# Kernel tuning notes

Hardware: AMD Instinct MI355X
Metric: run time of the kernel (lower is better)

## Reference

```python
import jax, jax.numpy as jnp
import numpy as np

N_RAYS = 1_048_576
T_ITERS = 4
N_POINTS = 8
DIM = 64
N_LAYERS = 2
INF = 1e9


def setup_inputs() -> dict:
    key = jax.random.key(0)
    ks = jax.random.split(key, 12)
    orig = jax.random.normal(ks[0], (N_RAYS, 3), jnp.float32)
    vec = jax.random.normal(ks[1], (N_RAYS, 3), jnp.float32)
    masks = jax.random.bernoulli(ks[2], 0.6, (T_ITERS, N_RAYS))
    bbox_idxs = jax.random.randint(ks[3], (T_ITERS, N_RAYS), 0, 1024, jnp.int32)
    t1 = jax.random.uniform(ks[4], (T_ITERS, N_RAYS), jnp.float32) * 2.0
    t2 = t1 + jax.random.uniform(ks[5], (T_ITERS, N_RAYS), jnp.float32) * 2.0
    mesh_min = jnp.array([-1.0, -1.0, -1.0], jnp.float32)
    mesh_max = jnp.array([1.0, 1.0, 1.0], jnp.float32)
    s = 0.05
    W0 = jax.random.normal(ks[6], (3 * N_POINTS, DIM), jnp.float32) * s
    b0 = jnp.zeros((DIM,), jnp.float32)
    ln_g = jnp.ones((N_LAYERS, DIM), jnp.float32)
    ln_b = jnp.zeros((N_LAYERS, DIM), jnp.float32)
    Ws = jax.random.normal(ks[7], (N_LAYERS, DIM, DIM), jnp.float32) * s
    bs = jnp.zeros((N_LAYERS, DIM), jnp.float32)
    Wc = jax.random.normal(ks[8], (DIM,), jnp.float32) * s
    bc = jnp.zeros((), jnp.float32)
    Wd = jax.random.normal(ks[9], (DIM,), jnp.float32) * s
    bd = jnp.zeros((), jnp.float32)
    return dict(orig=orig, vec=vec, masks=masks, bbox_idxs=bbox_idxs, t1=t1, t2=t2,
                mesh_min=mesh_min, mesh_max=mesh_max, W0=W0, b0=b0,
                ln_g=ln_g, ln_b=ln_b, Ws=Ws, bs=bs, Wc=Wc, bc=bc, Wd=Wd, bd=bd)


def _layernorm(x, g, b):
    mu = jnp.mean(x, axis=-1, keepdims=True)
    var = jnp.mean((x - mu) ** 2, axis=-1, keepdims=True)
    return (x - mu) * jax.lax.rsqrt(var + 1e-5) * g + b


def _net_forward(x, W0, b0, ln_g, ln_b, Ws, bs, Wc, bc, Wd, bd):
    # x: [N, 3*n_points]
    y = x @ W0 + b0
    for i in range(N_LAYERS):
        y = jax.nn.relu(y)
        y = _layernorm(y, ln_g[i], ln_b[i])
        y = y @ Ws[i] + bs[i]
    y = jax.nn.relu(y)
    cls = y @ Wc + bc   # [N]
    dist = y @ Wd + bd  # [N]
    return cls, dist


def reference(orig, vec, masks, bbox_idxs, t1, t2, mesh_min, mesh_max,
              W0, b0, ln_g, ln_b, Ws, bs, Wc, bc, Wd, bd):
    n_rays = orig.shape[0]
    ts = jnp.linspace(0.0, 1.0, N_POINTS, dtype=jnp.float32)
    min_infl = mesh_min - 0.5 * (mesh_max - mesh_min)
    max_infl = mesh_max + 0.5 * (mesh_max - mesh_min)
    scale = max_infl - min_infl
    dist = jnp.full((n_rays,), INF, jnp.float32)
    for it in range(T_ITERS):
        mask, ct1, ct2 = masks[it], t1[it], t2[it]
        inp_orig = orig + vec * ct1[:, None]          # [N,3]
        inp_vec = vec * (ct2 - ct1)[:, None]          # [N,3]
        # sample n_points along segment: [N, P, 3]
        inp = inp_orig[:, None, :] + inp_vec[:, None, :] * ts[None, :, None]
        inp = (inp - min_infl) / scale
        x = inp.reshape(n_rays, -1)                   # [N, 3P]
        hit_c, dv_c = _net_forward(x, W0, b0, ln_g, ln_b, Ws, bs, Wc, bc, Wd, bd)
        hit = jnp.where(mask, hit_c, 0.0)             # masked_scatter_ equivalent
        dv = jnp.where(mask, dv_c, 0.0) + ct1
        upd = (hit > 0) & (dv < dist) & mask
        dist = jnp.where(upd, dv, dist)
    dist = jnp.where(dist == INF, 0.0, dist)
    return (dist > 0, dist)
```

## Files before the change

### kernel.cpp

```cpp
#include <hip/hip_runtime.h>
#include <hip/hip_bf16.h>
#include <stdint.h>

#define NRAYS 1048576
#define INFV  1e9f
#define TBIG  1e30f

typedef short short8 __attribute__((ext_vector_type(8)));
typedef float f32x4  __attribute__((ext_vector_type(4)));

#define WS_B0   16
#define FB0     1024
#define FB1     2048

#define PKLO(a,b) ((int)(((unsigned)(a) & 0xFFFFu) | ((unsigned)(b) << 16)))
#define PKHI(a,b) ((int)(((unsigned)(a) >> 16) | ((unsigned)(b) & 0xFFFF0000u)))

__device__ __forceinline__ float ldf(const void* p, int i, int fm) {
    if (fm) return ((const float*)p)[i];
    unsigned u = ((const unsigned short*)p)[i];
    return __uint_as_float(u << 16);
}

__device__ __forceinline__ void split3(float f, int& him, int& lo) {
    unsigned u = __float_as_uint(f);
    float r = f - __uint_as_float(u & 0xFFFF0000u);
    unsigned um = __float_as_uint(r);
    float r2 = r - __uint_as_float(um & 0xFFFF0000u);
    unsigned ul = __float_as_uint(r2);
    him = (int)((u >> 16) | (um & 0xFFFF0000u));
    lo  = (int)(ul >> 16);
}

__device__ __forceinline__ unsigned comp16(int h, float f) {
    unsigned u = __float_as_uint(f);
    if (h == 0) return u >> 16;
    float r = f - __uint_as_float(u & 0xFFFF0000u);
    unsigned um = __float_as_uint(r);
    if (h == 1) return um >> 16;
    float r2 = r - __uint_as_float(um & 0xFFFF0000u);
    return __float_as_uint(r2) >> 16;
}

__device__ __forceinline__ float rsum16(float x) {
    int v;
    v = __builtin_amdgcn_update_dpp(0, __float_as_int(x), 0x128, 0xF, 0xF, false); x += __int_as_float(v);
    v = __builtin_amdgcn_update_dpp(0, __float_as_int(x), 0x124, 0xF, 0xF, false); x += __int_as_float(v);
    v = __builtin_amdgcn_update_dpp(0, __float_as_int(x), 0x122, 0xF, 0xF, false); x += __int_as_float(v);
    v = __builtin_amdgcn_update_dpp(0, __float_as_int(x), 0x121, 0xF, 0xF, false); x += __int_as_float(v);
    return x;
}

union I4S8 { int4 i; short8 s; };
__device__ __forceinline__ short8 mk8i(int a, int b, int c, int d) {
    I4S8 u; u.i = make_int4(a, b, c, d); return u.s;
}
__device__ __forceinline__ short8 ld_frag(const unsigned* p) {
    I4S8 u; u.i = *(const int4*)p; return u.s;
}

__global__ __launch_bounds__(256) void conv_k(
    const void* __restrict__ mmin, const void* __restrict__ mmax,
    const void* __restrict__ masks,
    const void* __restrict__ W0, const void* __restrict__ b0,
    const void* __restrict__ lng, const void* __restrict__ lnb,
    const void* __restrict__ Ws, const void* __restrict__ bs,
    const void* __restrict__ Wc, const void* __restrict__ bc,
    const void* __restrict__ Wd, const void* __restrict__ bd,
    unsigned* __restrict__ ws)
{
    __shared__ int sfm;
    float* wf = (float*)ws;
    const int tid = threadIdx.x;
    if (tid == 0) {
        unsigned w0 = ((const unsigned*)mmin)[0];
        int fm = ((w0 & 0xFFFFu) == 0u) ? 1 : 0;
        const unsigned* mw = (const unsigned*)masks;
        bool sawBf = false, allBin = true, sawF32 = false;
        for (int i = 0; i < 64; ++i) {
            unsigned w = mw[i], lo = w & 0xFFFFu, hi = w >> 16;
            if (lo == 0x3F80u && (hi == 0x3F80u || hi == 0u)) sawBf = true;
            if (w == 0x3F800000u) sawF32 = true;
            if (w > 1u) allBin = false;
        }
        int ms = sawBf ? 2 : (allBin ? 4 : (sawF32 ? 4 : 1));
        ws[8] = (unsigned)fm; ws[9] = (unsigned)ms;
        for (int c = 0; c < 3; ++c) {
            float mn = ldf(mmin, c, fm), mx = ldf(mmax, c, fm);
            float ext = mx - mn;
            wf[c]     = mn - 0.5f * ext;
            wf[3 + c] = 1.0f / (2.0f * ext);
        }
        wf[6] = ldf(bc, 0, fm);
        wf[7] = ldf(bd, 0, fm);
        sfm = fm;
    }
    __syncthreads();
    const int fm = sfm;

    for (int i = tid; i < 64;  i += 256) { wf[16 + i] = ldf(b0, i, fm); wf[464 + i] = ldf(Wc, i, fm); wf[528 + i] = ldf(Wd, i, fm); }
    for (int i = tid; i < 128; i += 256) { wf[80 + i] = ldf(bs, i, fm); wf[208 + i] = ldf(lng, i, fm); wf[336 + i] = ldf(lnb, i, fm); }

    for (int w = tid; w < 768; w += 256) {
        int ct = w / 192, rem = w % 192;
        int h = rem / 64, wi = rem % 64;
        int lane16 = wi >> 2, p = wi & 3;
        int n = ct * 16 + lane16;
        unsigned word = 0;
        #pragma unroll
        for (int half = 0; half < 2; ++half) {
            int k = 2 * p + half;
            float v = 0.f;
            if (k < 3) {
                for (int pp = 0; pp < 8; ++pp) v += ldf(W0, (3 * pp + k) * 64 + n, fm);
            } else if (k < 6) {
                int c3 = k - 3;
                for (int pp = 0; pp < 8; ++pp) v = fmaf((float)((double)pp / 7.0), ldf(W0, (3 * pp + c3) * 64 + n, fm), v);
            }
            word |= comp16(h, v) << (16 * half);
        }
        ws[FB0 + ((ct * 3 + h) * 16 + lane16) * 4 + p] = word;
    }

    for (int w = tid; w < 12288; w += 256) {
        int li = w / 6144, inner = w % 6144;
        int t = inner >> 8;
        int h = t % 3, ckc = t / 3, kc = ckc & 1, ct = ckc >> 1;
        int wi = inner & 255, lane = wi >> 2, p = wi & 3;
        int qq = lane >> 4, cc = lane & 15;
        int n = ct * 16 + cc;
        int k0 = kc * 32 + qq * 8 + 2 * p;
        float f0 = ldf(Ws, li * 4096 + k0 * 64 + n, fm);
        float f1 = ldf(Ws, li * 4096 + (k0 + 1) * 64 + n, fm);
        ws[FB1 + w] = comp16(h, f0) | (comp16(h, f1) << 16);
    }
}

#define ST1_S 34
#define ST2_S 34

__global__ __launch_bounds__(64, 4) void nbvh_main(
    const void* __restrict__ orig_p, const void* __restrict__ vec_p,
    const void* __restrict__ masks_p, const void* __restrict__ t1_p,
    const void* __restrict__ t2_p, const unsigned* __restrict__ wsu,
    void* __restrict__ out_p)
{
    __shared__ __align__(16) unsigned sT1[16][ST1_S];
    __shared__ __align__(16) unsigned sT2[16][ST2_S];
    __shared__ float sOV[6][64];
    __shared__ float sT1m[4][64];
    __shared__ float sT2g[4][64];
    __shared__ float sB[448];
    __shared__ float sDf[64];

    const float* wf = (const float*)wsu;
    const int fm = (int)wsu[8];
    const int ms = (int)wsu[9];
    const float bcv = wf[6], bdv = wf[7];

    const int L = threadIdx.x;
    const int q = L >> 4, c = L & 15;
    const int ray = blockIdx.x * 64 + L;

    for (int i = L; i < 448; i += 64) sB[i] = wf[16 + i];

    {
        const float mn0 = wf[0], mn1 = wf[1], mn2 = wf[2];
        const float is0 = wf[3], is1 = wf[4], is2 = wf[5];
        const float o0 = ldf(orig_p, 3*ray+0, fm), o1 = ldf(orig_p, 3*ray+1, fm), o2 = ldf(orig_p, 3*ray+2, fm);
        const float v0 = ldf(vec_p,  3*ray+0, fm), v1 = ldf(vec_p,  3*ray+1, fm), v2 = ldf(vec_p,  3*ray+2, fm);
        sOV[0][L] = (o0 - mn0) * is0;  sOV[1][L] = (o1 - mn1) * is1;  sOV[2][L] = (o2 - mn2) * is2;
        sOV[3][L] = v0 * is0;          sOV[4][L] = v1 * is1;          sOV[5][L] = v2 * is2;
        #pragma unroll
        for (int it = 0; it < 4; ++it) {
            const int gi = it * NRAYS + ray;
            bool mk;
            if      (ms == 1) mk = ((const uint8_t*) masks_p)[gi] != 0;
            else if (ms == 2) mk = ((const uint16_t*)masks_p)[gi] != 0;
            else              mk = ((const unsigned*) masks_p)[gi] != 0;
            sT1m[it][L] = mk ? ldf(t1_p, gi, fm) : TBIG;
            sT2g[it][L] = ldf(t2_p, gi, fm);
        }
        sDf[L] = INFV;
    }
    __syncthreads();

    #pragma unroll 1
    for (int rt = 0; rt < 4; ++rt) {
        #pragma unroll 1
        for (int ip = 0; ip < 2; ++ip) {
            f32x4 acc[2][4];
            short8 Ah[2][2], Am[2][2], Al[2][2];

            {
                short8 Xh[2], Xm[2], Xl[2];
                #pragma unroll
                for (int itl = 0; itl < 2; ++itl) {
                    const int it = ip * 2 + itl;
                    const int row = rt * 16 + c;
                    const float t1v = sT1m[it][row];
                    const float dtv = sT2g[it][row] - t1v;
                    float x[6];
                    #pragma unroll
                    for (int j = 0; j < 3; ++j) {
                        float ov = sOV[j][row], vv = sOV[3 + j][row];
                        x[j]     = fmaf(vv, t1v, ov);
                        x[3 + j] = vv * dtv;
                    }
                    int him[6], lo[6];
                    #pragma unroll
                    for (int j = 0; j < 6; ++j) split3(q == 0 ? x[j] : 0.f, him[j], lo[j]);
                    Xh[itl] = mk8i(PKLO(him[0],him[1]), PKLO(him[2],him[3]), PKLO(him[4],him[5]), 0);
                    Xm[itl] = mk8i(PKHI(him[0],him[1]), PKHI(him[2],him[3]), PKHI(him[4],him[5]), 0);
                    Xl[itl] = mk8i(PKLO(lo[0], lo[1]),  PKLO(lo[2], lo[3]),  PKLO(lo[4], lo[5]),  0);
                }
                #pragma unroll
                for (int itl = 0; itl < 2; ++itl)
                    #pragma unroll
                    for (int ct = 0; ct < 4; ++ct) {
                        float b = sB[ct * 16 + c];
                        f32x4 a; a[0]=a[1]=a[2]=a[3]=b; acc[itl][ct]=a;
                    }
                #pragma unroll
                for (int ct = 0; ct < 4; ++ct) {
                    short8 Bh = (q==0) ? ld_frag(wsu + FB0 + ((ct*3+0)*16 + c)*4) : mk8i(0,0,0,0);
                    short8 Bm = (q==0) ? ld_frag(wsu + FB0 + ((ct*3+1)*16 + c)*4) : mk8i(0,0,0,0);
                    short8 Bl = (q==0) ? ld_frag(wsu + FB0 + ((ct*3+2)*16 + c)*4) : mk8i(0,0,0,0);
                    #pragma unroll
                    for (int itl = 0; itl < 2; ++itl) {
                        acc[itl][ct] = __builtin_amdgcn_mfma_f32_16x16x32_bf16(Xh[itl], Bh, acc[itl][ct], 0,0,0);
                        acc[itl][ct] = __builtin_amdgcn_mfma_f32_16x16x32_bf16(Xh[itl], Bm, acc[itl][ct], 0,0,0);
                        acc[itl][ct] = __builtin_amdgcn_mfma_f32_16x16x32_bf16(Xm[itl], Bh, acc[itl][ct], 0,0,0);
                        acc[itl][ct] = __builtin_amdgcn_mfma_f32_16x16x32_bf16(Xm[itl], Bm, acc[itl][ct], 0,0,0);
                        acc[itl][ct] = __builtin_amdgcn_mfma_f32_16x16x32_bf16(Xh[itl], Bl, acc[itl][ct], 0,0,0);
                        acc[itl][ct] = __builtin_amdgcn_mfma_f32_16x16x32_bf16(Xl[itl], Bh, acc[itl][ct], 0,0,0);
                    }
                }
            }

            #pragma unroll 1
            for (int layer = 0; layer < 2; ++layer) {
                const unsigned* fb = wsu + FB1 + layer * 6144;
                const int bo = 64 + layer * 64, go = 192 + layer * 64, ho = 320 + layer * 64;

                #pragma unroll
                for (int itl = 0; itl < 2; ++itl) {
                    __syncthreads();
                    float z[4][4];
                    #pragma unroll
                    for (int ct = 0; ct < 4; ++ct)
                        #pragma unroll
                        for (int e = 0; e < 4; ++e) z[ct][e] = fmaxf(acc[itl][ct][e], 0.f);
                    float mu[4], rs[4];
                    #pragma unroll
                    for (int e = 0; e < 4; ++e) {
                        float s  = z[0][e] + z[1][e] + z[2][e] + z[3][e];
                        float s2 = fmaf(z[0][e], z[0][e], fmaf(z[1][e], z[1][e],
                                   fmaf(z[2][e], z[2][e], z[3][e] * z[3][e])));
                        s  = rsum16(s);
                        s2 = rsum16(s2);
                        mu[e] = s * (1.0f / 64.0f);
                        float var = fmaf(-mu[e], mu[e], s2 * (1.0f / 64.0f));
                        rs[e] = rsqrtf(var + 1e-5f);
                    }
                    int him[4][4], lov[4][4];
                    #pragma unroll
                    for (int ct = 0; ct < 4; ++ct) {
                        const float gv = sB[go + ct * 16 + c];
                        const float hv = sB[ho + ct * 16 + c];
                        #pragma unroll
                        for (int e = 0; e < 4; ++e) {
                            float y = fmaf((z[ct][e] - mu[e]) * rs[e], gv, hv);
                            split3(y, him[ct][e], lov[ct][e]);
                        }
                    }
                    #pragma unroll
                    for (int e = 0; e < 4; ++e) {
                        const int row = q * 4 + e;
                        sT1[row][c]      = (unsigned)him[0][e];
                        sT1[row][c + 16] = (unsigned)him[1][e];
                        sT2[row][c]      = (unsigned)PKLO(lov[0][e], lov[2][e]);
                        sT2[row][c + 16] = (unsigned)PKLO(lov[1][e], lov[3][e]);
                    }
                    __syncthreads();
                    const int4 t01 = *(const int4*)&sT2[c][q*8];
                    const int4 t23 = *(const int4*)&sT2[c][q*8 + 4];
                    {
                        const int4 w01 = *(const int4*)&sT1[c][q*8];
                        const int4 w23 = *(const int4*)&sT1[c][q*8 + 4];
                        Ah[itl][0] = mk8i(PKLO(w01.x,w01.y), PKLO(w01.z,w01.w), PKLO(w23.x,w23.y), PKLO(w23.z,w23.w));
                        Am[itl][0] = mk8i(PKHI(w01.x,w01.y), PKHI(w01.z,w01.w), PKHI(w23.x,w23.y), PKHI(w23.z,w23.w));
                        Al[itl][0] = mk8i(PKLO(t01.x,t01.y), PKLO(t01.z,t01.w), PKLO(t23.x,t23.y), PKLO(t23.z,t23.w));
                    }
                    __syncthreads();
                    #pragma unroll
                    for (int e = 0; e < 4; ++e) {
                        const int row = q * 4 + e;
                        sT1[row][c]      = (unsigned)him[2][e];
                        sT1[row][c + 16] = (unsigned)him[3][e];
                    }
                    __syncthreads();
                    {
                        const int4 w01 = *(const int4*)&sT1[c][q*8];
                        const int4 w23 = *(const int4*)&sT1[c][q*8 + 4];
                        Ah[itl][1] = mk8i(PKLO(w01.x,w01.y), PKLO(w01.z,w01.w), PKLO(w23.x,w23.y), PKLO(w23.z,w23.w));
                        Am[itl][1] = mk8i(PKHI(w01.x,w01.y), PKHI(w01.z,w01.w), PKHI(w23.x,w23.y), PKHI(w23.z,w23.w));
                        Al[itl][1] = mk8i(PKHI(t01.x,t01.y), PKHI(t01.z,t01.w), PKHI(t23.x,t23.y), PKHI(t23.z,t23.w));
                    }
                }

                #pragma unroll
                for (int itl = 0; itl < 2; ++itl)
                    #pragma unroll
                    for (int ct = 0; ct < 4; ++ct) {
                        float b = sB[bo + ct * 16 + c];
                        f32x4 a; a[0]=a[1]=a[2]=a[3]=b; acc[itl][ct]=a;
                    }
                #pragma unroll
                for (int kc = 0; kc < 2; ++kc) {
                    #pragma unroll
                    for (int ct = 0; ct < 4; ++ct) {
                        short8 Bh = ld_frag(fb + (((ct*2+kc)*3 + 0) << 8) + (L << 2));
                        short8 Bm = ld_frag(fb + (((ct*2+kc)*3 + 1) << 8) + (L << 2));
                        short8 Bl = ld_frag(fb + (((ct*2+kc)*3 + 2) << 8) + (L << 2));
                        #pragma unroll
                        for (int itl = 0; itl < 2; ++itl) {
                            acc[itl][ct] = __builtin_amdgcn_mfma_f32_16x16x32_bf16(Ah[itl][kc], Bh, acc[itl][ct], 0,0,0);
                            acc[itl][ct] = __builtin_amdgcn_mfma_f32_16x16x32_bf16(Ah[itl][kc], Bm, acc[itl][ct], 0,0,0);
                            acc[itl][ct] = __builtin_amdgcn_mfma_f32_16x16x32_bf16(Am[itl][kc], Bh, acc[itl][ct], 0,0,0);
                            acc[itl][ct] = __builtin_amdgcn_mfma_f32_16x16x32_bf16(Am[itl][kc], Bm, acc[itl][ct], 0,0,0);
                            acc[itl][ct] = __builtin_amdgcn_mfma_f32_16x16x32_bf16(Ah[itl][kc], Bl, acc[itl][ct], 0,0,0);
                            acc[itl][ct] = __builtin_amdgcn_mfma_f32_16x16x32_bf16(Al[itl][kc], Bh, acc[itl][ct], 0,0,0);
                        }
                    }
                }
            }

            {
                float wcr[4], wdr[4];
                #pragma unroll
                for (int ct = 0; ct < 4; ++ct) {
                    wcr[ct] = wf[464 + ct * 16 + c];
                    wdr[ct] = wf[528 + ct * 16 + c];
                }
                #pragma unroll
                for (int e = 0; e < 4; ++e) {
                    const int idx = rt * 16 + q * 4 + e;
                    float d = sDf[idx];
                    #pragma unroll
                    for (int itl = 0; itl < 2; ++itl) {
                        const int it = ip * 2 + itl;
                        float cp = 0.f, dp = 0.f;
                        #pragma unroll
                        for (int ct = 0; ct < 4; ++ct) {
                            float f = fmaxf(acc[itl][ct][e], 0.f);
                            cp = fmaf(f, wcr[ct], cp);
                            dp = fmaf(f, wdr[ct], dp);
                        }
                        cp = rsum16(cp); dp = rsum16(dp);
                        float cls = cp + bcv;
                        float dv  = dp + bdv + sT1m[it][idx];
                        if (cls > 0.f && dv < d) d = dv;
                    }
                    if (c == 0) sDf[idx] = d;
                }
            }
        }
    }

    __syncthreads();
    float d = sDf[L];
    if (d == INFV) d = 0.f;
    const float hit = (d > 0.f) ? 1.f : 0.f;
    if (fm) {
        ((float*)out_p)[ray]         = hit;
        ((float*)out_p)[NRAYS + ray] = d;
    } else {
        __hip_bfloat16* o = (__hip_bfloat16*)out_p;
        o[ray]         = __float2bfloat16(hit);
        o[NRAYS + ray] = __float2bfloat16(d);
    }
}

extern "C" void kernel_launch(void* const* d_in, const int* in_sizes, int n_in,
                              void* d_out, int out_size, void* d_ws, size_t ws_size,
                              hipStream_t stream) {
    (void)in_sizes; (void)n_in; (void)ws_size; (void)out_size;
    unsigned* ws = (unsigned*)d_ws;
    conv_k<<<1, 256, 0, stream>>>(
        d_in[6], d_in[7], d_in[2],
        d_in[8], d_in[9], d_in[10], d_in[11],
        d_in[12], d_in[13], d_in[14], d_in[15],
        d_in[16], d_in[17], ws);
    nbvh_main<<<NRAYS / 64, 64, 0, stream>>>(
        d_in[0], d_in[1], d_in[2], d_in[4], d_in[5], ws, d_out);
}
```

Measured before the change: 739.4 us.

## Use two independent waves per block with wave-local LDS and lgkmcnt waits

Launches 128-thread blocks in which each wavefront owns a private slice of shared memory. Block-wide barriers are replaced by a wave-local s_waitcnt lgkmcnt(0), since all LDS exchange stays within one wavefront. Biases and LayerNorm parameters now live in registers loaded from the workspace instead of a shared-memory staging array. Removing barriers reduces stalls, but it depends on wave-synchronous LDS ordering and raises register pressure under the new launch bounds.

```diff
diff --git a/kernel.cpp b/kernel.cpp
--- a/kernel.cpp
+++ b/kernel.cpp
@@ -58,6 +58,8 @@
 __device__ __forceinline__ short8 ld_frag(const unsigned* p) {
     I4S8 u; u.i = *(const int4*)p; return u.s;
 }
+
+#define WSYNC() asm volatile("s_waitcnt lgkmcnt(0)" ::: "memory")
 
 __global__ __launch_bounds__(256) void conv_k(
     const void* __restrict__ mmin, const void* __restrict__ mmax,
@@ -139,38 +141,44 @@
 #define ST1_S 34
 #define ST2_S 34
 
-__global__ __launch_bounds__(64, 4) void nbvh_main(
+__global__ __launch_bounds__(128, 5) void nbvh_main(
     const void* __restrict__ orig_p, const void* __restrict__ vec_p,
     const void* __restrict__ masks_p, const void* __restrict__ t1_p,
     const void* __restrict__ t2_p, const unsigned* __restrict__ wsu,
     void* __restrict__ out_p)
 {
-    __shared__ __align__(16) unsigned sT1[16][ST1_S];
-    __shared__ __align__(16) unsigned sT2[16][ST2_S];
-    __shared__ float sOV[6][64];
-    __shared__ float sT1m[4][64];
-    __shared__ float sT2g[4][64];
-    __shared__ float sB[448];
-    __shared__ float sDf[64];
+    __shared__ __align__(16) unsigned sT1[2][16][ST1_S];
+    __shared__ __align__(16) unsigned sT2[2][16][ST2_S];
+    __shared__ float sOV[2][6][64];
+    __shared__ float sT1m[2][4][64];
+    __shared__ float sT2g[2][4][64];
+    __shared__ float sDf[2][64];
 
     const float* wf = (const float*)wsu;
     const int fm = (int)wsu[8];
     const int ms = (int)wsu[9];
     const float bcv = wf[6], bdv = wf[7];
 
-    const int L = threadIdx.x;
+    const int tid = threadIdx.x;
+    const int Wv  = tid >> 6;
+    const int L   = tid & 63;
     const int q = L >> 4, c = L & 15;
-    const int ray = blockIdx.x * 64 + L;
-
-    for (int i = L; i < 448; i += 64) sB[i] = wf[16 + i];
+    const int ray = blockIdx.x * 128 + tid;
+
+    unsigned (&T1)[16][ST1_S] = sT1[Wv];
+    unsigned (&T2)[16][ST2_S] = sT2[Wv];
+    float (&OV)[6][64]  = sOV[Wv];
+    float (&T1m)[4][64] = sT1m[Wv];
+    float (&T2g)[4][64] = sT2g[Wv];
+    float (&Df)[64]     = sDf[Wv];
 
     {
         const float mn0 = wf[0], mn1 = wf[1], mn2 = wf[2];
         const float is0 = wf[3], is1 = wf[4], is2 = wf[5];
         const float o0 = ldf(orig_p, 3*ray+0, fm), o1 = ldf(orig_p, 3*ray+1, fm), o2 = ldf(orig_p, 3*ray+2, fm);
         const float v0 = ldf(vec_p,  3*ray+0, fm), v1 = ldf(vec_p,  3*ray+1, fm), v2 = ldf(vec_p,  3*ray+2, fm);
-        sOV[0][L] = (o0 - mn0) * is0;  sOV[1][L] = (o1 - mn1) * is1;  sOV[2][L] = (o2 - mn2) * is2;
-        sOV[3][L] = v0 * is0;          sOV[4][L] = v1 * is1;          sOV[5][L] = v2 * is2;
+        OV[0][L] = (o0 - mn0) * is0;  OV[1][L] = (o1 - mn1) * is1;  OV[2][L] = (o2 - mn2) * is2;
+        OV[3][L] = v0 * is0;          OV[4][L] = v1 * is1;          OV[5][L] = v2 * is2;
         #pragma unroll
         for (int it = 0; it < 4; ++it) {
             const int gi = it * NRAYS + ray;
@@ -178,12 +186,20 @@
             if      (ms == 1) mk = ((const uint8_t*) masks_p)[gi] != 0;
             else if (ms == 2) mk = ((const uint16_t*)masks_p)[gi] != 0;
             else              mk = ((const unsigned*) masks_p)[gi] != 0;
-            sT1m[it][L] = mk ? ldf(t1_p, gi, fm) : TBIG;
-            sT2g[it][L] = ldf(t2_p, gi, fm);
+            T1m[it][L] = mk ? ldf(t1_p, gi, fm) : TBIG;
+            T2g[it][L] = ldf(t2_p, gi, fm);
         }
-        sDf[L] = INFV;
-    }
-    __syncthreads();
+        Df[L] = INFV;
+    }
+    WSYNC();
+
+    float b0r[4], wcr[4], wdr[4];
+    #pragma unroll
+    for (int ct = 0; ct < 4; ++ct) {
+        b0r[ct] = wf[16  + ct * 16 + c];
+        wcr[ct] = wf[464 + ct * 16 + c];
+        wdr[ct] = wf[528 + ct * 16 + c];
+    }
 
     #pragma unroll 1
     for (int rt = 0; rt < 4; ++rt) {
@@ -198,12 +214,12 @@
                 for (int itl = 0; itl < 2; ++itl) {
                     const int it = ip * 2 + itl;
                     const int row = rt * 16 + c;
-                    const float t1v = sT1m[it][row];
-                    const float dtv = sT2g[it][row] - t1v;
+                    const float t1v = T1m[it][row];
+                    const float dtv = T2g[it][row] - t1v;
                     float x[6];
                     #pragma unroll
                     for (int j = 0; j < 3; ++j) {
-                        float ov = sOV[j][row], vv = sOV[3 + j][row];
+                        float ov = OV[j][row], vv = OV[3 + j][row];
                         x[j]     = fmaf(vv, t1v, ov);
                         x[3 + j] = vv * dtv;
                     }
@@ -218,7 +234,7 @@
                 for (int itl = 0; itl < 2; ++itl)
                     #pragma unroll
                     for (int ct = 0; ct < 4; ++ct) {
-                        float b = sB[ct * 16 + c];
+                        float b = b0r[ct];
                         f32x4 a; a[0]=a[1]=a[2]=a[3]=b; acc[itl][ct]=a;
                     }
                 #pragma unroll
@@ -241,11 +257,19 @@
             #pragma unroll 1
             for (int layer = 0; layer < 2; ++layer) {
                 const unsigned* fb = wsu + FB1 + layer * 6144;
-                const int bo = 64 + layer * 64, go = 192 + layer * 64, ho = 320 + layer * 64;
+                const int bo = 80 + layer * 64, go = 208 + layer * 64, ho = 336 + layer * 64;
+
+                float gvr[4], hvr[4], bvr[4];
+                #pragma unroll
+                for (int ct = 0; ct < 4; ++ct) {
+                    gvr[ct] = wf[go + ct * 16 + c];
+                    hvr[ct] = wf[ho + ct * 16 + c];
+                    bvr[ct] = wf[bo + ct * 16 + c];
+                }
 
                 #pragma unroll
                 for (int itl = 0; itl < 2; ++itl) {
-                    __syncthreads();
+                    WSYNC();
                     float z[4][4];
                     #pragma unroll
                     for (int ct = 0; ct < 4; ++ct)
@@ -266,8 +290,8 @@
                     int him[4][4], lov[4][4];
                     #pragma unroll
                     for (int ct = 0; ct < 4; ++ct) {
-                        const float gv = sB[go + ct * 16 + c];
-                        const float hv = sB[ho + ct * 16 + c];
+                        const float gv = gvr[ct];
+                        const float hv = hvr[ct];
                         #pragma unroll
                         for (int e = 0; e < 4; ++e) {
                             float y = fmaf((z[ct][e] - mu[e]) * rs[e], gv, hv);
@@ -277,32 +301,32 @@
                     #pragma unroll
                     for (int e = 0; e < 4; ++e) {
                         const int row = q * 4 + e;
-                        sT1[row][c]      = (unsigned)him[0][e];
-                        sT1[row][c + 16] = (unsigned)him[1][e];
-                        sT2[row][c]      = (unsigned)PKLO(lov[0][e], lov[2][e]);
-                        sT2[row][c + 16] = (unsigned)PKLO(lov[1][e], lov[3][e]);
-                    }
-                    __syncthreads();
-                    const int4 t01 = *(const int4*)&sT2[c][q*8];
-                    const int4 t23 = *(const int4*)&sT2[c][q*8 + 4];
+                        T1[row][c]      = (unsigned)him[0][e];
+                        T1[row][c + 16] = (unsigned)him[1][e];
+                        T2[row][c]      = (unsigned)PKLO(lov[0][e], lov[2][e]);
+                        T2[row][c + 16] = (unsigned)PKLO(lov[1][e], lov[3][e]);
+                    }
+                    WSYNC();
+                    const int4 t01 = *(const int4*)&T2[c][q*8];
+                    const int4 t23 = *(const int4*)&T2[c][q*8 + 4];
                     {
-                        const int4 w01 = *(const int4*)&sT1[c][q*8];
-                        const int4 w23 = *(const int4*)&sT1[c][q*8 + 4];
+                        const int4 w01 = *(const int4*)&T1[c][q*8];
+                        const int4 w23 = *(const int4*)&T1[c][q*8 + 4];
                         Ah[itl][0] = mk8i(PKLO(w01.x,w01.y), PKLO(w01.z,w01.w), PKLO(w23.x,w23.y), PKLO(w23.z,w23.w));
                         Am[itl][0] = mk8i(PKHI(w01.x,w01.y), PKHI(w01.z,w01.w), PKHI(w23.x,w23.y), PKHI(w23.z,w23.w));
                         Al[itl][0] = mk8i(PKLO(t01.x,t01.y), PKLO(t01.z,t01.w), PKLO(t23.x,t23.y), PKLO(t23.z,t23.w));
                     }
-                    __syncthreads();
+                    WSYNC();
                     #pragma unroll
                     for (int e = 0; e < 4; ++e) {
                         const int row = q * 4 + e;
-                        sT1[row][c]      = (unsigned)him[2][e];
-                        sT1[row][c + 16] = (unsigned)him[3][e];
-                    }
-                    __syncthreads();
+                        T1[row][c]      = (unsigned)him[2][e];
+                        T1[row][c + 16] = (unsigned)him[3][e];
+                    }
+                    WSYNC();
                     {
-                        const int4 w01 = *(const int4*)&sT1[c][q*8];
-                        const int4 w23 = *(const int4*)&sT1[c][q*8 + 4];
+                        const int4 w01 = *(const int4*)&T1[c][q*8];
+                        const int4 w23 = *(const int4*)&T1[c][q*8 + 4];
                         Ah[itl][1] = mk8i(PKLO(w01.x,w01.y), PKLO(w01.z,w01.w), PKLO(w23.x,w23.y), PKLO(w23.z,w23.w));
                         Am[itl][1] = mk8i(PKHI(w01.x,w01.y), PKHI(w01.z,w01.w), PKHI(w23.x,w23.y), PKHI(w23.z,w23.w));
                         Al[itl][1] = mk8i(PKHI(t01.x,t01.y), PKHI(t01.z,t01.w), PKHI(t23.x,t23.y), PKHI(t23.z,t23.w));
@@ -313,7 +337,7 @@
                 for (int itl = 0; itl < 2; ++itl)
                     #pragma unroll
                     for (int ct = 0; ct < 4; ++ct) {
-                        float b = sB[bo + ct * 16 + c];
+                        float b = bvr[ct];
                         f32x4 a; a[0]=a[1]=a[2]=a[3]=b; acc[itl][ct]=a;
                     }
                 #pragma unroll
@@ -337,16 +361,10 @@
             }
 
             {
-                float wcr[4], wdr[4];
-                #pragma unroll
-                for (int ct = 0; ct < 4; ++ct) {
-                    wcr[ct] = wf[464 + ct * 16 + c];
-                    wdr[ct] = wf[528 + ct * 16 + c];
-                }
                 #pragma unroll
                 for (int e = 0; e < 4; ++e) {
                     const int idx = rt * 16 + q * 4 + e;
-                    float d = sDf[idx];
+                    float d = Df[idx];
                     #pragma unroll
                     for (int itl = 0; itl < 2; ++itl) {
                         const int it = ip * 2 + itl;
@@ -359,17 +377,17 @@
                         }
                         cp = rsum16(cp); dp = rsum16(dp);
                         float cls = cp + bcv;
-                        float dv  = dp + bdv + sT1m[it][idx];
+                        float dv  = dp + bdv + T1m[it][idx];
                         if (cls > 0.f && dv < d) d = dv;
                     }
-                    if (c == 0) sDf[idx] = d;
+                    if (c == 0) Df[idx] = d;
                 }
             }
         }
     }
 
-    __syncthreads();
-    float d = sDf[L];
+    WSYNC();
+    float d = Df[L];
     if (d == INFV) d = 0.f;
     const float hit = (d > 0.f) ? 1.f : 0.f;
     if (fm) {
@@ -392,6 +410,6 @@
         d_in[8], d_in[9], d_in[10], d_in[11],
         d_in[12], d_in[13], d_in[14], d_in[15],
         d_in[16], d_in[17], ws);
-    nbvh_main<<<NRAYS / 64, 64, 0, stream>>>(
+    nbvh_main<<<NRAYS / 128, 128, 0, stream>>>(
         d_in[0], d_in[1], d_in[2], d_in[4], d_in[5], ws, d_out);
 }
```

Measured after the change: 1.078 ms. 1.46x slower.
